# Kernel tuning notes

Hardware: AMD Instinct MI355X
Metric: run time of the kernel (lower is better)

The kernel has to match this reference:

```python
import jax, jax.numpy as jnp
import numpy as np

N_NODES = 50000
N_EDGES = 600000
D = 128
HIDDEN = 128
N_GRAPHS = 128
N_CLASSES = 10
N_STACKED = 3  # num_layers - 1


def setup_inputs() -> dict:
    key = jax.random.key(0)
    ks = jax.random.split(key, 12)
    s = 1.0 / np.sqrt(HIDDEN)
    inp = {
        "x": jax.random.normal(ks[0], (N_NODES, D), dtype=jnp.float32),
        "edge_index": jax.random.randint(ks[1], (2, N_EDGES), 0, N_NODES, dtype=jnp.int64),
        "batch": jnp.sort(jax.random.randint(ks[2], (N_NODES,), 0, N_GRAPHS, dtype=jnp.int64)),
        "W1": jax.random.normal(ks[3], (D, HIDDEN), dtype=jnp.float32) * s,
        "R1": jax.random.normal(ks[4], (D, HIDDEN), dtype=jnp.float32) * s,
        "b1": jnp.zeros((HIDDEN,), dtype=jnp.float32),
        "Wc": jax.random.normal(ks[5], (N_STACKED, HIDDEN, HIDDEN), dtype=jnp.float32) * s,
        "Rc": jax.random.normal(ks[6], (N_STACKED, HIDDEN, HIDDEN), dtype=jnp.float32) * s,
        "bc": jnp.zeros((N_STACKED, HIDDEN), dtype=jnp.float32),
        "lin1_w": jax.random.normal(ks[7], (HIDDEN, HIDDEN), dtype=jnp.float32) * s,
        "lin1_b": jnp.zeros((HIDDEN,), dtype=jnp.float32),
        "lin2_w": jax.random.normal(ks[8], (HIDDEN, N_CLASSES), dtype=jnp.float32) * s,
        "lin2_b": jnp.zeros((N_CLASSES,), dtype=jnp.float32),
    }
    return inp


def _gcn_norm(edge_index, n_nodes):
    # symmetric GCN normalization coeffs per edge (edge_weight=None -> ones)
    src, dst = edge_index[0], edge_index[1]
    ones = jnp.ones((edge_index.shape[1],), dtype=jnp.float32)
    deg = jax.ops.segment_sum(ones, dst, num_segments=n_nodes)
    dinv = jnp.where(deg > 0, jax.lax.rsqrt(jnp.maximum(deg, 1.0)), 0.0)
    return dinv[src] * dinv[dst]


def _gcs(x, src, dst, norm, W, R, b):
    # GCN aggregation on transformed features + linear skip (root) connection
    h = x @ W                                   # [N, H]
    msg = h[src] * norm[:, None]                # gather + scale, [E, H]
    agg = jax.ops.segment_sum(msg, dst, num_segments=x.shape[0])
    return agg + x @ R + b


def reference(x, edge_index, batch, W1, R1, b1, Wc, Rc, bc,
              lin1_w, lin1_b, lin2_w, lin2_b):
    src, dst = edge_index[0], edge_index[1]
    norm = _gcn_norm(edge_index, x.shape[0])

    h = jax.nn.relu(_gcs(x, src, dst, norm, W1, R1, b1))
    for i in range(N_STACKED):
        h = jax.nn.relu(_gcs(h, src, dst, norm, Wc[i], Rc[i], bc[i]))
    last = h

    # global mean pool over graphs
    sums = jax.ops.segment_sum(h, batch, num_segments=N_GRAPHS)
    cnts = jax.ops.segment_sum(jnp.ones((h.shape[0],), h.dtype), batch,
                               num_segments=N_GRAPHS)
    pooled = sums / jnp.maximum(cnts, 1.0)[:, None]

    g = jax.nn.relu(pooled @ lin1_w + lin1_b)   # dropout is identity in eval mode
    logits = g @ lin2_w + lin2_b
    return jax.nn.log_softmax(logits, axis=-1), last
```

## Files before the change

kernel.cpp:

```cpp
#include <hip/hip_runtime.h>

#define N_NODES  50000
#define N_EDGES  600000
#define DIM      128
#define N_GRAPHS 128
#define N_CLASSES 10
#define NB_SCAN  196
#define ZWORDS   1700000
#define NZB4     1661


typedef __bf16 bf16x8 __attribute__((ext_vector_type(8)));
typedef float  f32x4  __attribute__((ext_vector_type(4)));

__device__ inline unsigned short f2bf(float f) {
  union { float f; unsigned int i; } u; u.f = f;
  unsigned int r = u.i + 0x7fff + ((u.i >> 16) & 1);
  return (unsigned short)(r >> 16);
}
__device__ inline float bf2f(unsigned short s) {
  union { unsigned int i; float f; } u; u.i = ((unsigned int)s) << 16;
  return u.f;
}
__device__ inline bf16x8 pack8(float4 lo, float4 hi) {
  union { bf16x8 v; unsigned short s[8]; } u;
  u.s[0] = f2bf(lo.x); u.s[1] = f2bf(lo.y); u.s[2] = f2bf(lo.z); u.s[3] = f2bf(lo.w);
  u.s[4] = f2bf(hi.x); u.s[5] = f2bf(hi.y); u.s[6] = f2bf(hi.z); u.s[7] = f2bf(hi.w);
  return u.v;
}
__device__ inline bf16x8 zero8() {
  union { bf16x8 v; unsigned short s[8]; } u;
#pragma unroll
  for (int j = 0; j < 8; ++j) u.s[j] = 0;
  return u.v;
}


__global__ __launch_bounds__(256) void k_prep(float4* __restrict__ z4,
                                              const float* __restrict__ W1,
                                              const float* __restrict__ R1,
                                              const float* __restrict__ Wc,
                                              const float* __restrict__ Rc,
                                              unsigned short* __restrict__ pk) {
  if (blockIdx.x < NZB4) {
    int i = blockIdx.x * 256 + threadIdx.x;
    if (i < ZWORDS / 4) z4[i] = make_float4(0.f, 0.f, 0.f, 0.f);
    return;
  }
  int pb = blockIdx.x - NZB4;
  int mm = pb >> 3, sub = pb & 7;
  const float* src = (mm == 0) ? W1
                   : (mm < 4)  ? Wc + (size_t)(mm - 1) * DIM * DIM
                   : (mm == 4) ? R1
                               : Rc + (size_t)(mm - 5) * DIM * DIM;
  int idx = sub * 256 + threadIdx.x;
  int lane = idx & 63;
  int kc   = (idx >> 6) & 3;
  int nt   = idx >> 8;
  int col  = nt * 16 + (lane & 15);
  int k0   = kc * 32 + (lane >> 4) * 8;
  unsigned short* dst = pk + (size_t)mm * 16384 + (size_t)idx * 8;
  ushort4 u;
  u.x = f2bf(src[(k0 + 0) * DIM + col]);
  u.y = f2bf(src[(k0 + 1) * DIM + col]);
  u.z = f2bf(src[(k0 + 2) * DIM + col]);
  u.w = f2bf(src[(k0 + 3) * DIM + col]);
  *(ushort4*)&dst[0] = u;
  u.x = f2bf(src[(k0 + 4) * DIM + col]);
  u.y = f2bf(src[(k0 + 5) * DIM + col]);
  u.z = f2bf(src[(k0 + 6) * DIM + col]);
  u.w = f2bf(src[(k0 + 7) * DIM + col]);
  *(ushort4*)&dst[4] = u;
}


__global__ __launch_bounds__(256) void k_deg(const int* __restrict__ ei,
                                             int* __restrict__ deg) {
  int e = blockIdx.x * 256 + threadIdx.x;
  if (e < N_EDGES) atomicAdd(&deg[ei[N_EDGES + e]], 1);
}

__global__ __launch_bounds__(256) void k_dinvsum(const int* __restrict__ deg,
                                                 float* __restrict__ dinv,
                                                 int* __restrict__ bsum) {
  int i = blockIdx.x * 256 + threadIdx.x;
  int t = threadIdx.x;
  int d = (i < N_NODES) ? deg[i] : 0;
  if (i < N_NODES) dinv[i] = (d > 0) ? rsqrtf((float)d) : 0.f;
  int dp = (d + 7) & ~7;
  __shared__ int tmp[256];
  tmp[t] = dp;
  __syncthreads();
  for (int off = 128; off > 0; off >>= 1) {
    if (t < off) tmp[t] += tmp[t + off];
    __syncthreads();
  }
  if (t == 0) bsum[blockIdx.x] = tmp[0];
}

__global__ __launch_bounds__(256) void k_bscan(const int* __restrict__ bsum,
                                               int* __restrict__ boff,
                                               int* __restrict__ rowp) {
  int t = threadIdx.x;
  int v = (t < NB_SCAN) ? bsum[t] : 0;
  __shared__ int tmp[256];
  tmp[t] = v;
  __syncthreads();
  for (int off = 1; off < 256; off <<= 1) {
    int add = (t >= off) ? tmp[t - off] : 0;
    __syncthreads();
    tmp[t] += add;
    __syncthreads();
  }
  boff[t] = tmp[t] - v;
  if (t == 255) rowp[N_NODES] = tmp[255];
}

__global__ __launch_bounds__(256) void k_rowp(const int* __restrict__ deg,
                                              const int* __restrict__ boff,
                                              int* __restrict__ rowp) {
  int i = blockIdx.x * 256 + threadIdx.x;
  int t = threadIdx.x;
  int dp = (i < N_NODES) ? ((deg[i] + 7) & ~7) : 0;
  __shared__ int tmp[256];
  tmp[t] = dp;
  __syncthreads();
  for (int off = 1; off < 256; off <<= 1) {
    int add = (t >= off) ? tmp[t - off] : 0;
    __syncthreads();
    tmp[t] += add;
    __syncthreads();
  }
  if (i < N_NODES) rowp[i] = boff[blockIdx.x] + tmp[t] - dp;
}

__global__ __launch_bounds__(256) void k_fill(const int* __restrict__ ei,
                                              const int* __restrict__ rowp,
                                              int* __restrict__ cnt,
                                              const float* __restrict__ dinv,
                                              int2* __restrict__ epk) {
  int e = blockIdx.x * 256 + threadIdx.x;
  if (e < N_EDGES) {
    int s = ei[e];
    int d = ei[N_EDGES + e];
    int p = rowp[d] + atomicAdd(&cnt[d], 1);
    epk[p] = make_int2(s, __float_as_int(dinv[s] * dinv[d]));
  }
}


__global__ __launch_bounds__(256) void k_gemm0(const float* __restrict__ xf,
                                               const unsigned short* __restrict__ pkW,
                                               const unsigned short* __restrict__ pkR,
                                               const float* __restrict__ bv,
                                               unsigned short* __restrict__ hwb,
                                               unsigned short* __restrict__ skipb) {
  const int tid  = threadIdx.x;
  const int wave = tid >> 6, lane = tid & 63;
  const int m = lane & 15, q = lane >> 4;
  const int rbase = blockIdx.x * 64 + wave * 16;
  const int arow  = rbase + m;
  const bool aok  = arow < N_NODES;

  bf16x8 a[4];
#pragma unroll
  for (int kc = 0; kc < 4; ++kc) {
    float4 lo = make_float4(0.f, 0.f, 0.f, 0.f);
    float4 hi = make_float4(0.f, 0.f, 0.f, 0.f);
    if (aok) {
      lo = *(const float4*)&xf[arow * DIM + kc * 32 + q * 8];
      hi = *(const float4*)&xf[arow * DIM + kc * 32 + q * 8 + 4];
    }
    a[kc] = pack8(lo, hi);
  }

  f32x4 acc[16];
#pragma unroll
  for (int t = 0; t < 16; ++t) acc[t] = (f32x4){0.f, 0.f, 0.f, 0.f};

#pragma unroll
  for (int nt = 0; nt < 8; ++nt) {
    const unsigned short* pw = pkW + ((size_t)(nt * 4) * 64 + lane) * 8;
    const unsigned short* pr = pkR + ((size_t)(nt * 4) * 64 + lane) * 8;
#pragma unroll
    for (int kc = 0; kc < 4; ++kc) {
      bf16x8 bW = *(const bf16x8*)(pw + (size_t)kc * 64 * 8);
      acc[nt] = __builtin_amdgcn_mfma_f32_16x16x32_bf16(a[kc], bW, acc[nt], 0, 0, 0);
    }
#pragma unroll
    for (int kc = 0; kc < 4; ++kc) {
      bf16x8 bR = *(const bf16x8*)(pr + (size_t)kc * 64 * 8);
      acc[8 + nt] = __builtin_amdgcn_mfma_f32_16x16x32_bf16(a[kc], bR, acc[8 + nt], 0, 0, 0);
    }
  }

#pragma unroll
  for (int nt = 0; nt < 8; ++nt) {
    int col = nt * 16 + m;
    float bias = bv[col];
#pragma unroll
    for (int rg = 0; rg < 4; ++rg) {
      int row = rbase + q * 4 + rg;
      if (row < N_NODES) {
        hwb[row * DIM + col]   = f2bf(acc[nt][rg]);
        skipb[row * DIM + col] = f2bf(acc[8 + nt][rg] + bias);
      }
    }
  }
}


__global__ __launch_bounds__(256) void k_gath(const unsigned short* __restrict__ hin,
                                              const int* __restrict__ rowp,
                                              const int2* __restrict__ epk,
                                              const unsigned short* __restrict__ skipb,
                                              unsigned short* __restrict__ gout) {
  int n = blockIdx.x * 8 + (threadIdx.x >> 5);
  if (n >= N_NODES) return;
  int l4 = (threadIdx.x & 31) * 4;
  int e0 = rowp[n], e1 = rowp[n + 1];
  ushort4 s = *(const ushort4*)&skipb[n * DIM + l4];
  float4 accA = make_float4(0.f, 0.f, 0.f, 0.f);
  float4 accB = make_float4(0.f, 0.f, 0.f, 0.f);
  for (int ea = e0, eb = e1 - 4; ea < eb; ea += 4, eb -= 4) {
    int4 p0 = *(const int4*)&epk[ea];
    int4 p1 = *(const int4*)&epk[ea + 2];
    int4 p2 = *(const int4*)&epk[eb];
    int4 p3 = *(const int4*)&epk[eb + 2];
    ushort4 u0 = *(const ushort4*)&hin[p0.x * DIM + l4];
    ushort4 u1 = *(const ushort4*)&hin[p0.z * DIM + l4];
    ushort4 u2 = *(const ushort4*)&hin[p1.x * DIM + l4];
    ushort4 u3 = *(const ushort4*)&hin[p1.z * DIM + l4];
    ushort4 u4 = *(const ushort4*)&hin[p2.x * DIM + l4];
    ushort4 u5 = *(const ushort4*)&hin[p2.z * DIM + l4];
    ushort4 u6 = *(const ushort4*)&hin[p3.x * DIM + l4];
    ushort4 u7 = *(const ushort4*)&hin[p3.z * DIM + l4];
    float w0 = __int_as_float(p0.y), w1 = __int_as_float(p0.w);
    float w2 = __int_as_float(p1.y), w3 = __int_as_float(p1.w);
    float w4 = __int_as_float(p2.y), w5 = __int_as_float(p2.w);
    float w6 = __int_as_float(p3.y), w7 = __int_as_float(p3.w);
    accA.x = fmaf(w0, bf2f(u0.x), fmaf(w1, bf2f(u1.x), fmaf(w2, bf2f(u2.x), fmaf(w3, bf2f(u3.x), accA.x))));
    accA.y = fmaf(w0, bf2f(u0.y), fmaf(w1, bf2f(u1.y), fmaf(w2, bf2f(u2.y), fmaf(w3, bf2f(u3.y), accA.y))));
    accA.z = fmaf(w0, bf2f(u0.z), fmaf(w1, bf2f(u1.z), fmaf(w2, bf2f(u2.z), fmaf(w3, bf2f(u3.z), accA.z))));
    accA.w = fmaf(w0, bf2f(u0.w), fmaf(w1, bf2f(u1.w), fmaf(w2, bf2f(u2.w), fmaf(w3, bf2f(u3.w), accA.w))));
    accB.x = fmaf(w4, bf2f(u4.x), fmaf(w5, bf2f(u5.x), fmaf(w6, bf2f(u6.x), fmaf(w7, bf2f(u7.x), accB.x))));
    accB.y = fmaf(w4, bf2f(u4.y), fmaf(w5, bf2f(u5.y), fmaf(w6, bf2f(u6.y), fmaf(w7, bf2f(u7.y), accB.y))));
    accB.z = fmaf(w4, bf2f(u4.z), fmaf(w5, bf2f(u5.z), fmaf(w6, bf2f(u6.z), fmaf(w7, bf2f(u7.z), accB.z))));
    accB.w = fmaf(w4, bf2f(u4.w), fmaf(w5, bf2f(u5.w), fmaf(w6, bf2f(u6.w), fmaf(w7, bf2f(u7.w), accB.w))));
  }
  ushort4 o;
  o.x = f2bf(fmaxf(accA.x + accB.x + bf2f(s.x), 0.f));
  o.y = f2bf(fmaxf(accA.y + accB.y + bf2f(s.y), 0.f));
  o.z = f2bf(fmaxf(accA.z + accB.z + bf2f(s.z), 0.f));
  o.w = f2bf(fmaxf(accA.w + accB.w + bf2f(s.w), 0.f));
  *(ushort4*)&gout[n * DIM + l4] = o;
}


template<bool LAST>
__global__ __launch_bounds__(256) void k_gemmb(unsigned short* __restrict__ gio,
                                               const unsigned short* __restrict__ pkW,
                                               const unsigned short* __restrict__ pkR,
                                               const float* __restrict__ bv,
                                               unsigned short* __restrict__ skipb,
                                               float* __restrict__ skipf) {
  const int tid  = threadIdx.x;
  const int wave = tid >> 6, lane = tid & 63;
  const int m = lane & 15, q = lane >> 4;
  const int rbase = blockIdx.x * 64 + wave * 16;
  const int arow  = rbase + m;
  const bool aok  = arow < N_NODES;

  bf16x8 a[4];
#pragma unroll
  for (int kc = 0; kc < 4; ++kc)
    a[kc] = aok ? *(const bf16x8*)&gio[arow * DIM + kc * 32 + q * 8] : zero8();

  f32x4 acc[16];
#pragma unroll
  for (int t = 0; t < 16; ++t) acc[t] = (f32x4){0.f, 0.f, 0.f, 0.f};

#pragma unroll
  for (int nt = 0; nt < 8; ++nt) {
    const unsigned short* pw = pkW + ((size_t)(nt * 4) * 64 + lane) * 8;
    const unsigned short* pr = pkR + ((size_t)(nt * 4) * 64 + lane) * 8;
#pragma unroll
    for (int kc = 0; kc < 4; ++kc) {
      bf16x8 bW = *(const bf16x8*)(pw + (size_t)kc * 64 * 8);
      acc[nt] = __builtin_amdgcn_mfma_f32_16x16x32_bf16(a[kc], bW, acc[nt], 0, 0, 0);
    }
#pragma unroll
    for (int kc = 0; kc < 4; ++kc) {
      bf16x8 bR = *(const bf16x8*)(pr + (size_t)kc * 64 * 8);
      acc[8 + nt] = __builtin_amdgcn_mfma_f32_16x16x32_bf16(a[kc], bR, acc[8 + nt], 0, 0, 0);
    }
  }

#pragma unroll
  for (int nt = 0; nt < 8; ++nt) {
    int col = nt * 16 + m;
    float bias = bv[col];
#pragma unroll
    for (int rg = 0; rg < 4; ++rg) {
      int row = rbase + q * 4 + rg;
      if (row < N_NODES) {
        gio[row * DIM + col] = f2bf(acc[nt][rg]);
        float v = acc[8 + nt][rg] + bias;
        if (LAST) skipf[row * DIM + col] = v;
        else      skipb[row * DIM + col] = f2bf(v);
      }
    }
  }
}


__global__ __launch_bounds__(256) void k_aggF(const unsigned short* __restrict__ hwb,
                                              const int* __restrict__ rowp,
                                              const int2* __restrict__ epk,
                                              float* __restrict__ actf) {
  int n = blockIdx.x * 8 + (threadIdx.x >> 5);
  if (n >= N_NODES) return;
  int l4 = (threadIdx.x & 31) * 4;
  int e0 = rowp[n], e1 = rowp[n + 1];
  float4 s = *(const float4*)&actf[n * DIM + l4];
  float4 accA = make_float4(0.f, 0.f, 0.f, 0.f);
  float4 accB = make_float4(0.f, 0.f, 0.f, 0.f);
  for (int ea = e0, eb = e1 - 4; ea < eb; ea += 4, eb -= 4) {
    int4 p0 = *(const int4*)&epk[ea];
    int4 p1 = *(const int4*)&epk[ea + 2];
    int4 p2 = *(const int4*)&epk[eb];
    int4 p3 = *(const int4*)&epk[eb + 2];
    ushort4 u0 = *(const ushort4*)&hwb[p0.x * DIM + l4];
    ushort4 u1 = *(const ushort4*)&hwb[p0.z * DIM + l4];
    ushort4 u2 = *(const ushort4*)&hwb[p1.x * DIM + l4];
    ushort4 u3 = *(const ushort4*)&hwb[p1.z * DIM + l4];
    ushort4 u4 = *(const ushort4*)&hwb[p2.x * DIM + l4];
    ushort4 u5 = *(const ushort4*)&hwb[p2.z * DIM + l4];
    ushort4 u6 = *(const ushort4*)&hwb[p3.x * DIM + l4];
    ushort4 u7 = *(const ushort4*)&hwb[p3.z * DIM + l4];
    float w0 = __int_as_float(p0.y), w1 = __int_as_float(p0.w);
    float w2 = __int_as_float(p1.y), w3 = __int_as_float(p1.w);
    float w4 = __int_as_float(p2.y), w5 = __int_as_float(p2.w);
    float w6 = __int_as_float(p3.y), w7 = __int_as_float(p3.w);
    accA.x = fmaf(w0, bf2f(u0.x), fmaf(w1, bf2f(u1.x), fmaf(w2, bf2f(u2.x), fmaf(w3, bf2f(u3.x), accA.x))));
    accA.y = fmaf(w0, bf2f(u0.y), fmaf(w1, bf2f(u1.y), fmaf(w2, bf2f(u2.y), fmaf(w3, bf2f(u3.y), accA.y))));
    accA.z = fmaf(w0, bf2f(u0.z), fmaf(w1, bf2f(u1.z), fmaf(w2, bf2f(u2.z), fmaf(w3, bf2f(u3.z), accA.z))));
    accA.w = fmaf(w0, bf2f(u0.w), fmaf(w1, bf2f(u1.w), fmaf(w2, bf2f(u2.w), fmaf(w3, bf2f(u3.w), accA.w))));
    accB.x = fmaf(w4, bf2f(u4.x), fmaf(w5, bf2f(u5.x), fmaf(w6, bf2f(u6.x), fmaf(w7, bf2f(u7.x), accB.x))));
    accB.y = fmaf(w4, bf2f(u4.y), fmaf(w5, bf2f(u5.y), fmaf(w6, bf2f(u6.y), fmaf(w7, bf2f(u7.y), accB.y))));
    accB.z = fmaf(w4, bf2f(u4.z), fmaf(w5, bf2f(u5.z), fmaf(w6, bf2f(u6.z), fmaf(w7, bf2f(u7.z), accB.z))));
    accB.w = fmaf(w4, bf2f(u4.w), fmaf(w5, bf2f(u5.w), fmaf(w6, bf2f(u6.w), fmaf(w7, bf2f(u7.w), accB.w))));
  }
  float4 o;
  o.x = fmaxf(accA.x + accB.x + s.x, 0.f);
  o.y = fmaxf(accA.y + accB.y + s.y, 0.f);
  o.z = fmaxf(accA.z + accB.z + s.z, 0.f);
  o.w = fmaxf(accA.w + accB.w + s.w, 0.f);
  *(float4*)&actf[n * DIM + l4] = o;
}


__global__ __launch_bounds__(1024) void k_pool2(const float* __restrict__ h,
                                                const int* __restrict__ batch,
                                                float* __restrict__ pooled) {
  int g = blockIdx.x;
  int t = threadIdx.x;
  __shared__ int sb[2];
  if (t < 2) {
    int target = g + t;
    int lo = 0, hi = N_NODES;
    while (lo < hi) {
      int mid = (lo + hi) >> 1;
      if (batch[mid] < target) lo = mid + 1; else hi = mid;
    }
    sb[t] = lo;
  }
  __syncthreads();
  int start = sb[0], end = sb[1];
  int c = t & 127, rg = t >> 7;
  float acc = 0.f;
  for (int r = start + rg; r < end; r += 8) acc += h[r * DIM + c];
  __shared__ float sp[8][DIM];
  sp[rg][c] = acc;
  __syncthreads();
  if (rg == 0) {
    float tot = acc;
#pragma unroll
    for (int i = 1; i < 8; ++i) tot += sp[i][c];
    float cnt = fmaxf((float)(end - start), 1.f);
    pooled[g * DIM + c] = tot / cnt;
  }
}


__global__ __launch_bounds__(128) void k_mlp1(const float* __restrict__ pooled,
                                              const float* __restrict__ w,
                                              const float* __restrict__ bias,
                                              float* __restrict__ g1) {
  int g = blockIdx.x, t = threadIdx.x;
  __shared__ float sp[DIM];
  sp[t] = pooled[g * DIM + t];
  __syncthreads();
  float acc = bias[t];
#pragma unroll 4
  for (int k = 0; k < DIM; ++k) acc = fmaf(sp[k], w[k * DIM + t], acc);
  g1[g * DIM + t] = fmaxf(acc, 0.f);
}

__global__ __launch_bounds__(128) void k_mlp2(const float* __restrict__ g1,
                                              const float* __restrict__ w,
                                              const float* __restrict__ bias,
                                              float* __restrict__ out) {
  int g = threadIdx.x;
  float l[N_CLASSES];
#pragma unroll
  for (int c = 0; c < N_CLASSES; ++c) l[c] = bias[c];
  for (int k = 0; k < DIM; ++k) {
    float gv = g1[g * DIM + k];
#pragma unroll
    for (int c = 0; c < N_CLASSES; ++c) l[c] = fmaf(gv, w[k * N_CLASSES + c], l[c]);
  }
  float m = l[0];
#pragma unroll
  for (int c = 1; c < N_CLASSES; ++c) m = fmaxf(m, l[c]);
  float s = 0.f;
#pragma unroll
  for (int c = 0; c < N_CLASSES; ++c) s += expf(l[c] - m);
  float lse = logf(s) + m;
#pragma unroll
  for (int c = 0; c < N_CLASSES; ++c) out[g * N_CLASSES + c] = l[c] - lse;
}


extern "C" void kernel_launch(void* const* d_in, const int* in_sizes, int n_in,
                              void* d_out, int out_size, void* d_ws, size_t ws_size,
                              hipStream_t stream) {
  const float* x     = (const float*)d_in[0];
  const int* ei      = (const int*)d_in[1];
  const int* batch   = (const int*)d_in[2];
  const float* W1  = (const float*)d_in[3];
  const float* R1  = (const float*)d_in[4];
  const float* b1  = (const float*)d_in[5];
  const float* Wc  = (const float*)d_in[6];
  const float* Rc  = (const float*)d_in[7];
  const float* bc  = (const float*)d_in[8];
  const float* l1w = (const float*)d_in[9];
  const float* l1b = (const float*)d_in[10];
  const float* l2w = (const float*)d_in[11];
  const float* l2b = (const float*)d_in[12];

  float* out   = (float*)d_out;
  float* dlast = out + N_GRAPHS * N_CLASSES;

  float* ws = (float*)d_ws;
  unsigned short* X = (unsigned short*)ws;
  unsigned short* Y = (unsigned short*)(ws + 3203072);
  unsigned short* S = (unsigned short*)(ws + 6406144);
  int*   deg   = (int*)(ws + 9609216);
  int*   cnt   = (int*)(ws + 9659216);
  int2*  epk   = (int2*)(ws + 9709216);
  float* dinv  = ws + 11309216;
  int*   rowp  = (int*)(ws + 11359216);
  float* pooled= ws + 11409232;
  float* g1    = ws + 11425616;
  unsigned short* pk = (unsigned short*)(ws + 11442000);
  int*   bsum  = (int*)(ws + 11507536);
  int*   boff  = (int*)(ws + 11507792);

  k_prep<<<NZB4 + 64, 256, 0, stream>>>((float4*)(ws + 9609216), W1, R1, Wc, Rc, pk);
  k_deg <<<(N_EDGES + 255) / 256, 256, 0, stream>>>(ei, deg);
  k_dinvsum<<<NB_SCAN, 256, 0, stream>>>(deg, dinv, bsum);
  k_bscan<<<1, 256, 0, stream>>>(bsum, boff, rowp);
  k_rowp<<<NB_SCAN, 256, 0, stream>>>(deg, boff, rowp);
  k_fill<<<(N_EDGES + 255) / 256, 256, 0, stream>>>(ei, rowp, cnt, dinv, epk);

  const int NGB = (N_NODES + 63) / 64;
  const int NAB = (N_NODES + 7) / 8;

  k_gemm0<<<NGB, 256, 0, stream>>>(x, pk + 0 * 16384, pk + 4 * 16384, b1, X, S);
  k_gath <<<NAB, 256, 0, stream>>>(X, rowp, epk, S, Y);
  k_gemmb<false><<<NGB, 256, 0, stream>>>(Y, pk + 1 * 16384, pk + 5 * 16384,
                                          bc + 0 * DIM, S, nullptr);
  k_gath <<<NAB, 256, 0, stream>>>(Y, rowp, epk, S, X);
  k_gemmb<false><<<NGB, 256, 0, stream>>>(X, pk + 2 * 16384, pk + 6 * 16384,
                                          bc + 1 * DIM, S, nullptr);
  k_gath <<<NAB, 256, 0, stream>>>(X, rowp, epk, S, Y);
  k_gemmb<true><<<NGB, 256, 0, stream>>>(Y, pk + 3 * 16384, pk + 7 * 16384,
                                         bc + 2 * DIM, S, dlast);
  k_aggF<<<NAB, 256, 0, stream>>>(Y, rowp, epk, dlast);

  k_pool2<<<N_GRAPHS, 1024, 0, stream>>>(dlast, batch, pooled);
  k_mlp1<<<N_GRAPHS, 128, 0, stream>>>(pooled, l1w, l1b, g1);
  k_mlp2<<<1, N_GRAPHS, 0, stream>>>(g1, l2w, l2b, out);
}
```

Measured before the change: 386.0 us.

## Fuse global mean-pool partial sums into final aggregation kernel via atomics

The last aggregation kernel now also reduces its 8 output rows per block into per-graph partial sums in shared memory. It flushes those sums with atomicAdd into a zeroed psum buffer, and the zeroing is added to the prep kernel. The separate pooling kernel is removed, and the MLP kernel divides by the node counts it gets from a binary search on batch. This avoids re-reading the full final activation matrix and saves one launch. The cost is an extra __syncthreads, atomic contention on the 128x128 sum buffer, and a float summation order that is no longer deterministic.

```diff
diff --git a/kernel.cpp b/kernel.cpp
--- a/kernel.cpp
+++ b/kernel.cpp
@@ -8,6 +8,7 @@
 #define NB_SCAN  196
 #define ZWORDS   1700000
 #define NZB4     1661
+#define NPB      16
 
 
 typedef __bf16 bf16x8 __attribute__((ext_vector_type(8)));
@@ -37,6 +38,7 @@
 
 
 __global__ __launch_bounds__(256) void k_prep(float4* __restrict__ z4,
+                                              float4* __restrict__ pz,
                                               const float* __restrict__ W1,
                                               const float* __restrict__ R1,
                                               const float* __restrict__ Wc,
@@ -47,7 +49,12 @@
     if (i < ZWORDS / 4) z4[i] = make_float4(0.f, 0.f, 0.f, 0.f);
     return;
   }
-  int pb = blockIdx.x - NZB4;
+  if (blockIdx.x < NZB4 + NPB) {
+    int i = (blockIdx.x - NZB4) * 256 + threadIdx.x;
+    pz[i] = make_float4(0.f, 0.f, 0.f, 0.f);
+    return;
+  }
+  int pb = blockIdx.x - NZB4 - NPB;
   int mm = pb >> 3, sub = pb & 7;
   const float* src = (mm == 0) ? W1
                    : (mm < 4)  ? Wc + (size_t)(mm - 1) * DIM * DIM
@@ -317,10 +324,16 @@
 __global__ __launch_bounds__(256) void k_aggF(const unsigned short* __restrict__ hwb,
                                               const int* __restrict__ rowp,
                                               const int2* __restrict__ epk,
-                                              float* __restrict__ actf) {
-  int n = blockIdx.x * 8 + (threadIdx.x >> 5);
-  if (n >= N_NODES) return;
-  int l4 = (threadIdx.x & 31) * 4;
+                                              const int* __restrict__ batch,
+                                              float* __restrict__ actf,
+                                              float* __restrict__ psum) {
+  __shared__ float sp[8][132];
+  __shared__ int gb[8];
+  const int tid = threadIdx.x;
+  const int n0 = blockIdx.x * 8;
+  const int n = n0 + (tid >> 5);
+  const int l4 = (tid & 31) * 4;
+  if (tid < 8) gb[tid] = batch[n0 + tid];
   int e0 = rowp[n], e1 = rowp[n + 1];
   float4 s = *(const float4*)&actf[n * DIM + l4];
   float4 accA = make_float4(0.f, 0.f, 0.f, 0.f);
@@ -357,14 +370,30 @@
   o.z = fmaxf(accA.z + accB.z + s.z, 0.f);
   o.w = fmaxf(accA.w + accB.w + s.w, 0.f);
   *(float4*)&actf[n * DIM + l4] = o;
-}
-
-
-__global__ __launch_bounds__(1024) void k_pool2(const float* __restrict__ h,
-                                                const int* __restrict__ batch,
-                                                float* __restrict__ pooled) {
-  int g = blockIdx.x;
-  int t = threadIdx.x;
+  int r = tid >> 5;
+  sp[r][l4 + 0] = o.x; sp[r][l4 + 1] = o.y;
+  sp[r][l4 + 2] = o.z; sp[r][l4 + 3] = o.w;
+  __syncthreads();
+  if (tid < DIM) {
+    int gprev = gb[0];
+    float acc = 0.f;
+#pragma unroll
+    for (int rr = 0; rr < 8; ++rr) {
+      int g = gb[rr];
+      if (g != gprev) { atomicAdd(&psum[gprev * DIM + tid], acc); acc = 0.f; gprev = g; }
+      acc += sp[rr][tid];
+    }
+    atomicAdd(&psum[gprev * DIM + tid], acc);
+  }
+}
+
+
+__global__ __launch_bounds__(128) void k_mlp1(const float* __restrict__ psum,
+                                              const int* __restrict__ batch,
+                                              const float* __restrict__ w,
+                                              const float* __restrict__ bias,
+                                              float* __restrict__ g1) {
+  int g = blockIdx.x, t = threadIdx.x;
   __shared__ int sb[2];
   if (t < 2) {
     int target = g + t;
@@ -376,30 +405,9 @@
     sb[t] = lo;
   }
   __syncthreads();
-  int start = sb[0], end = sb[1];
-  int c = t & 127, rg = t >> 7;
-  float acc = 0.f;
-  for (int r = start + rg; r < end; r += 8) acc += h[r * DIM + c];
-  __shared__ float sp[8][DIM];
-  sp[rg][c] = acc;
-  __syncthreads();
-  if (rg == 0) {
-    float tot = acc;
-#pragma unroll
-    for (int i = 1; i < 8; ++i) tot += sp[i][c];
-    float cnt = fmaxf((float)(end - start), 1.f);
-    pooled[g * DIM + c] = tot / cnt;
-  }
-}
-
-
-__global__ __launch_bounds__(128) void k_mlp1(const float* __restrict__ pooled,
-                                              const float* __restrict__ w,
-                                              const float* __restrict__ bias,
-                                              float* __restrict__ g1) {
-  int g = blockIdx.x, t = threadIdx.x;
+  float cnt = fmaxf((float)(sb[1] - sb[0]), 1.f);
   __shared__ float sp[DIM];
-  sp[t] = pooled[g * DIM + t];
+  sp[t] = psum[g * DIM + t] / cnt;
   __syncthreads();
   float acc = bias[t];
 #pragma unroll 4
@@ -461,13 +469,14 @@
   int2*  epk   = (int2*)(ws + 9709216);
   float* dinv  = ws + 11309216;
   int*   rowp  = (int*)(ws + 11359216);
-  float* pooled= ws + 11409232;
+  float* psum  = ws + 11409232;
   float* g1    = ws + 11425616;
   unsigned short* pk = (unsigned short*)(ws + 11442000);
   int*   bsum  = (int*)(ws + 11507536);
   int*   boff  = (int*)(ws + 11507792);
 
-  k_prep<<<NZB4 + 64, 256, 0, stream>>>((float4*)(ws + 9609216), W1, R1, Wc, Rc, pk);
+  k_prep<<<NZB4 + NPB + 64, 256, 0, stream>>>((float4*)(ws + 9609216),
+                                              (float4*)psum, W1, R1, Wc, Rc, pk);
   k_deg <<<(N_EDGES + 255) / 256, 256, 0, stream>>>(ei, deg);
   k_dinvsum<<<NB_SCAN, 256, 0, stream>>>(deg, dinv, bsum);
   k_bscan<<<1, 256, 0, stream>>>(bsum, boff, rowp);
@@ -487,9 +496,8 @@
   k_gath <<<NAB, 256, 0, stream>>>(X, rowp, epk, S, Y);
   k_gemmb<true><<<NGB, 256, 0, stream>>>(Y, pk + 3 * 16384, pk + 7 * 16384,
                                          bc + 2 * DIM, S, dlast);
-  k_aggF<<<NAB, 256, 0, stream>>>(Y, rowp, epk, dlast);
-
-  k_pool2<<<N_GRAPHS, 1024, 0, stream>>>(dlast, batch, pooled);
-  k_mlp1<<<N_GRAPHS, 128, 0, stream>>>(pooled, l1w, l1b, g1);
+  k_aggF<<<NAB, 256, 0, stream>>>(Y, rowp, epk, batch, dlast, psum);
+
+  k_mlp1<<<N_GRAPHS, 128, 0, stream>>>(psum, batch, l1w, l1b, g1);
   k_mlp2<<<1, N_GRAPHS, 0, stream>>>(g1, l2w, l2b, out);
 }
```

Measured after the change: 372.2 us. -3.6%, faster.
